# Kernel tuning notes

Measured on AMD Instinct MI355X. Metric: run time of the kernel, lower is better.

The kernel has to match this reference:

```python
import jax, jax.numpy as jnp
import numpy as np

BETA = 0.25  # commitment-loss weight (kwargs['beta'])


def setup_inputs() -> dict:
    key = jax.random.key(0)
    k1, k2 = jax.random.split(key)
    B, C, H, W = 16, 256, 64, 64
    K = 2048
    feats = jax.random.normal(k1, (B, C, H, W), dtype=jnp.float32)
    # nn.Embedding init: uniform(-1/n_codewords, 1/codeword_dim)
    codebook = jax.random.uniform(k2, (K, C), minval=-1.0 / K, maxval=1.0 / C,
                                  dtype=jnp.float32)
    return {"feats": feats, "codebook": codebook}


def reference(feats, codebook):
    B, C, H, W = feats.shape
    K = codebook.shape[0]
    z = jnp.transpose(feats, (0, 2, 3, 1))          # [B,H,W,C]
    zf = z.reshape(-1, C)                            # [N,C], N=B*H*W
    # squared-euclidean distances via ||z||^2 + ||e||^2 - 2 z.e : [N,K]
    d = (jnp.sum(zf * zf, axis=1, keepdims=True)
         + jnp.sum(codebook * codebook, axis=1)
         - 2.0 * (zf @ codebook.T))
    min_encoding_indices = jnp.argmin(d, axis=1)     # [N]
    mat_id_probs = jax.nn.softmax(-jnp.abs(d), axis=1)  # [N,K]
    z_q = codebook[min_encoding_indices].reshape(z.shape)  # [B,H,W,C]
    loss = (BETA * jnp.mean((jax.lax.stop_gradient(z_q) - z) ** 2)
            + jnp.mean((z_q - jax.lax.stop_gradient(z)) ** 2))
    # straight-through estimator
    z_q_st = z + jax.lax.stop_gradient(z_q - z)
    z_q_out = jnp.transpose(z_q_st, (0, 3, 1, 2))    # [B,C,H,W]
    idx_out = min_encoding_indices.reshape(B, H, W)
    probs_out = jnp.transpose(mat_id_probs.reshape(B, H, W, K), (0, 3, 1, 2))
    return z_q_out, idx_out, loss, probs_out
```

## Files before the change

kernel.cpp:

```cpp
#include <hip/hip_runtime.h>

#define HW 4096
#define CC 256
#define KK 2048
#define BB 16
#define NN (BB*HW)

#define ZQ_SZ   (BB*CC*HW)
#define IDX_OFF ZQ_SZ
#define LOSS_OFF (IDX_OFF + NN)
#define PROBS_OFF (LOSS_OFF + 1)

#define EH_OFF 0
#define EE_OFF 262144
#define ZZ_OFF 264192

#define TAU 0.01f
#define CAND_CAP 2048
#define KTC 64
#define KT_N 32

typedef short bf16x8 __attribute__((ext_vector_type(8)));
typedef float f32x16 __attribute__((ext_vector_type(16)));

__device__ __forceinline__ unsigned short bf16rn(float x){
  unsigned u = __float_as_uint(x);
  return (unsigned short)((u + 0x7fffu + ((u >> 16) & 1u)) >> 16);
}

template<int STRIDE>
__device__ __forceinline__ float np_sumsq256(const float* __restrict__ a){
  float res0 = 0.f, res1 = 0.f;
  #pragma unroll
  for (int h = 0; h < 2; h++){
    const float* p = a + (size_t)h * 128 * STRIDE;
    float r[8];
    #pragma unroll
    for (int j = 0; j < 8; j++){ float x = p[(size_t)j * STRIDE]; r[j] = __fmul_rn(x, x); }
    for (int i = 8; i < 128; i += 8){
      #pragma unroll
      for (int j = 0; j < 8; j++){
        float x = p[(size_t)(i + j) * STRIDE];
        r[j] = __fadd_rn(r[j], __fmul_rn(x, x));
      }
    }
    float s = __fadd_rn(__fadd_rn(__fadd_rn(r[0], r[1]), __fadd_rn(r[2], r[3])),
                        __fadd_rn(__fadd_rn(r[4], r[5]), __fadd_rn(r[6], r[7])));
    if (h == 0) res0 = s; else res1 = s;
  }
  return __fadd_rn(res0, res1);
}

__global__ void k_prep2(const float* __restrict__ cb, float* __restrict__ out){
  const int k = blockIdx.x * 256 + threadIdx.x;
  unsigned short* eh = (unsigned short*)(out + EH_OFF);
  const float* row = cb + (size_t)k * CC;
  for (int c = 0; c < CC; c++) eh[k * CC + c] = bf16rn(row[c]);
  out[EE_OFF + k] = np_sumsq256<1>(row);
}

__global__ void k_zz(const float* __restrict__ feats, float* __restrict__ out){
  const int n = blockIdx.x * 256 + threadIdx.x;
  const int b = n >> 12, hw = n & 4095;
  out[ZZ_OFF + n] = np_sumsq256<HW>(feats + (size_t)b * CC * HW + hw);
}

__global__ __launch_bounds__(512, 2)
void k_mfma(const float* __restrict__ feats, const float* __restrict__ cb,
            float* __restrict__ out){
  __shared__ __align__(16) unsigned char lds_e[32768];
  __shared__ float ee_lds[KK];
  __shared__ float pbuf[8448];
  __shared__ unsigned long long rowkey[256];
  __shared__ int cand[CAND_CAP];
  __shared__ int cand_n;
  __shared__ float lsum;

  const int t = threadIdx.x;
  const int w = t >> 6, l = t & 63;
  const int blk = blockIdx.x;
  const int n0 = blk * 256;
  const int bi = n0 >> 12;
  const int hw0 = n0 & 4095;
  const int grp = l >> 5;
  const int code_l = l & 31;
  const int myhw = hw0 + w * 32 + (l & 31);
  const int wb = w * 1056;

  for (int i = t; i < KK; i += 512) ee_lds[i] = out[EE_OFF + i];
  if (t < 256) rowkey[t] = ~0ull;
  if (t == 0){ cand_n = 0; lsum = 0.f; }

  bf16x8 ah[16];
  {
    const float* zb = feats + (size_t)bi * CC * HW + myhw;
    #pragma unroll
    for (int cs = 0; cs < 16; ++cs){
      #pragma unroll
      for (int j = 0; j < 8; ++j){
        int c = cs * 16 + grp * 8 + j;
        ah[cs][j] = (short)bf16rn(zb[(size_t)c * HW]);
      }
    }
  }

  const unsigned short* ehg = (const unsigned short*)(out + EH_OFF);
  float4 stg[4];

#define VLOAD(KT) { \
    _Pragma("unroll") \
    for (int i_ = 0; i_ < 4; ++i_){ \
      int ix_ = i_ * 512 + t; \
      int cd_ = ix_ & 63; \
      int g_  = (ix_ >> 6) & 1; \
      int cs_ = ix_ >> 7; \
      stg[i_] = *(const float4*)(ehg + (size_t)((KT) * KTC + cd_) * CC + cs_ * 16 + g_ * 8); \
    } }

#define DSWRITE() { \
    _Pragma("unroll") \
    for (int i_ = 0; i_ < 4; ++i_) *(float4*)(lds_e + (i_ * 512 + t) * 16) = stg[i_]; }

#define COMPUTE() \
    _Pragma("unroll") \
    for (int ii = 0; ii < 16; ++ii){ accA[ii] = 0.f; accB[ii] = 0.f; accC[ii] = 0.f; accD[ii] = 0.f; } \
    _Pragma("unroll") \
    for (int cs = 0; cs < 16; ++cs){ \
      const unsigned char* bp_ = lds_e + (size_t)(cs * 2 + grp) * 1024 + code_l * 16; \
      bf16x8 b0_ = *(const bf16x8*)(bp_); \
      bf16x8 b1_ = *(const bf16x8*)(bp_ + 512); \
      if (cs & 1){ \
        accB = __builtin_amdgcn_mfma_f32_32x32x16_bf16(ah[cs], b0_, accB, 0, 0, 0); \
        accD = __builtin_amdgcn_mfma_f32_32x32x16_bf16(ah[cs], b1_, accD, 0, 0, 0); \
      } else { \
        accA = __builtin_amdgcn_mfma_f32_32x32x16_bf16(ah[cs], b0_, accA, 0, 0, 0); \
        accC = __builtin_amdgcn_mfma_f32_32x32x16_bf16(ah[cs], b1_, accC, 0, 0, 0); \
      } \
    }

  f32x16 accA, accB, accC, accD;
  float m_[16], sum_[16];
  #pragma unroll
  for (int r = 0; r < 16; ++r){ m_[r] = 3e38f; sum_[r] = 0.f; }

  VLOAD(0);
  for (int kt = 0; kt < KT_N; ++kt){
    __syncthreads();
    DSWRITE();
    __syncthreads();
    if (kt < KT_N - 1) VLOAD(kt + 1);
    COMPUTE();
    float eev0 = ee_lds[kt * KTC + code_l];
    float eev1 = ee_lds[kt * KTC + 32 + code_l];
    #pragma unroll
    for (int r = 0; r < 16; ++r){
      float s0 = eev0 - 2.f * (accA[r] + accB[r]);
      float s1 = eev1 - 2.f * (accC[r] + accD[r]);
      m_[r] = fminf(m_[r], fminf(s0, s1));
      sum_[r] += __expf(-s0) + __expf(-s1);
    }
  }

  #pragma unroll
  for (int r = 0; r < 16; ++r){
    float m = m_[r], ss = sum_[r];
    #pragma unroll
    for (int off = 1; off < 32; off <<= 1){
      m = fminf(m, __shfl_xor(m, off));
      ss += __shfl_xor(ss, off);
    }
    m_[r] = m; sum_[r] = 1.f / ss;
  }

  VLOAD(0);
  for (int kt = 0; kt < KT_N; ++kt){
    __syncthreads();
    DSWRITE();
    __syncthreads();
    if (kt < KT_N - 1) VLOAD(kt + 1);
    COMPUTE();
    float eev0 = ee_lds[kt * KTC + code_l];
    float eev1 = ee_lds[kt * KTC + 32 + code_l];
    const int row = l & 31, hi = l >> 5;
    #pragma unroll
    for (int cf = 0; cf < 2; ++cf){
      #pragma unroll
      for (int r = 0; r < 16; ++r){
        float a = cf ? (accC[r] + accD[r]) : (accA[r] + accB[r]);
        float s = (cf ? eev1 : eev0) - 2.f * a;
        float p = __expf(-s) * sum_[r];
        int rloc = (r & 3) + 8 * (r >> 2) + 4 * grp;
        pbuf[wb + code_l * 33 + rloc] = p;
        if (s <= m_[r] + TAU){
          int slot = atomicAdd(&cand_n, 1);
          if (slot < CAND_CAP) cand[slot] = ((w * 32 + rloc) << 16) | (kt * KTC + cf * 32 + code_l);
        }
      }
      #pragma unroll
      for (int i = 0; i < 16; ++i){
        int codel = 2 * i + hi;
        float pv = pbuf[wb + codel * 33 + row];
        out[(size_t)PROBS_OFF + (size_t)(bi * KK + kt * KTC + cf * 32 + codel) * HW + hw0 + w * 32 + row] = pv;
      }
    }
  }
  __syncthreads();

  int nc = cand_n; if (nc > CAND_CAP) nc = CAND_CAP;
  for (int i = t; i < nc; i += 512){
    int rc = cand[i];
    int rl = rc >> 16, code = rc & 0xffff;
    int n = n0 + rl;
    const float* zp = feats + (size_t)(n >> 12) * CC * HW + (n & 4095);
    const float* ep = cb + (size_t)code * CC;
    float a = 0.f;
    #pragma unroll 8
    for (int c = 0; c < CC; ++c) a = __builtin_fmaf(zp[(size_t)c * HW], ep[c], a);
    float t1 = __fadd_rn(out[ZZ_OFF + n], ee_lds[code]);
    float d = __fadd_rn(t1, -2.f * a);
    unsigned long long key = ((unsigned long long)__float_as_uint(d) << 32) | (unsigned)code;
    atomicMin(&rowkey[rl], key);
  }
  __syncthreads();

  if (t < 256) out[IDX_OFF + n0 + t] = (float)(int)(rowkey[t] & 0xffffffffu);

  {
    int rl = w * 32 + (l & 31);
    int code = (int)(rowkey[rl] & 0xffffffffu);
    const float* ep = cb + (size_t)code * CC;
    int n = n0 + rl;
    const float* zp = feats + (size_t)(n >> 12) * CC * HW + (n & 4095);
    float s = 0.f;
    int c0 = grp * 128;
    for (int c = c0; c < c0 + 128; ++c){
      float dz = ep[c] - zp[(size_t)c * HW];
      s = __builtin_fmaf(dz, dz, s);
    }
    s += __shfl_xor(s, 32);
    if (grp == 0) atomicAdd(&lsum, s);
  }
  __syncthreads();
  if (t == 0) atomicAdd(out + LOSS_OFF, lsum * (1.25f / 16777216.f));
}

__global__ void k_zq(const float* __restrict__ cb, float* __restrict__ out){
  const int f4 = blockIdx.x * 256 + threadIdx.x;
  const int f = f4 * 4;
  const int b = f >> 20;
  const int rem = f & 1048575;
  const int c = rem >> 12;
  const int hw = rem & 4095;
  const int n = b * HW + hw;
  const float* idxf = out + IDX_OFF;
  float4 iv = *(const float4*)(idxf + n);
  float4 o;
  o.x = cb[(size_t)((int)iv.x) * CC + c];
  o.y = cb[(size_t)((int)iv.y) * CC + c];
  o.z = cb[(size_t)((int)iv.z) * CC + c];
  o.w = cb[(size_t)((int)iv.w) * CC + c];
  *(float4*)(out + f) = o;
}

extern "C" void kernel_launch(void* const* d_in, const int* in_sizes, int n_in,
                              void* d_out, int out_size, void* d_ws, size_t ws_size,
                              hipStream_t stream){
  const float* feats = (const float*)d_in[0];
  const float* cb    = (const float*)d_in[1];
  float* out = (float*)d_out;

  (void)hipMemsetAsync(out + LOSS_OFF, 0, sizeof(float), stream);
  hipLaunchKernelGGL(k_prep2, dim3(8),     dim3(256), 0, stream, cb, out);
  hipLaunchKernelGGL(k_zz,    dim3(256),   dim3(256), 0, stream, feats, out);
  hipLaunchKernelGGL(k_mfma,  dim3(256),   dim3(512), 0, stream, feats, cb, out);
  hipLaunchKernelGGL(k_zq,    dim3(16384), dim3(256), 0, stream, cb, out);
}
```

Before: 500.8 us.

## Double-buffer codebook tiles, swap MFMA operands, store probs directly, drop zz kernel

The two passes over codebook tiles are merged into one 64-iteration loop that uses a double-buffered LDS tile, so each iteration needs one barrier instead of two. MFMA operands are swapped so each lane holds a single row's distances, which removes the 32-lane shuffle reductions and the pbuf LDS transpose. Probabilities are written straight to global memory with nontemporal stores. The separate k_zz kernel is removed and ||z||^2 is recomputed per candidate instead. The extra buffer raises LDS use, and the direct stores may coalesce differently than the old transposed writes.

```diff
diff --git a/kernel.cpp b/kernel.cpp
--- a/kernel.cpp
+++ b/kernel.cpp
@@ -13,7 +13,6 @@
 
 #define EH_OFF 0
 #define EE_OFF 262144
-#define ZZ_OFF 264192
 
 #define TAU 0.01f
 #define CAND_CAP 2048
@@ -59,18 +58,11 @@
   out[EE_OFF + k] = np_sumsq256<1>(row);
 }
 
-__global__ void k_zz(const float* __restrict__ feats, float* __restrict__ out){
-  const int n = blockIdx.x * 256 + threadIdx.x;
-  const int b = n >> 12, hw = n & 4095;
-  out[ZZ_OFF + n] = np_sumsq256<HW>(feats + (size_t)b * CC * HW + hw);
-}
-
 __global__ __launch_bounds__(512, 2)
 void k_mfma(const float* __restrict__ feats, const float* __restrict__ cb,
             float* __restrict__ out){
-  __shared__ __align__(16) unsigned char lds_e[32768];
+  __shared__ __align__(16) unsigned char lds_e[2][32768];
   __shared__ float ee_lds[KK];
-  __shared__ float pbuf[8448];
   __shared__ unsigned long long rowkey[256];
   __shared__ int cand[CAND_CAP];
   __shared__ int cand_n;
@@ -78,14 +70,13 @@
 
   const int t = threadIdx.x;
   const int w = t >> 6, l = t & 63;
-  const int blk = blockIdx.x;
-  const int n0 = blk * 256;
+  const int n0 = blockIdx.x * 256;
   const int bi = n0 >> 12;
   const int hw0 = n0 & 4095;
   const int grp = l >> 5;
   const int code_l = l & 31;
-  const int myhw = hw0 + w * 32 + (l & 31);
-  const int wb = w * 1056;
+  const int zrow = l & 31;
+  const int myhw = hw0 + w * 32 + zrow;
 
   for (int i = t; i < KK; i += 512) ee_lds[i] = out[EE_OFF + i];
   if (t < 256) rowkey[t] = ~0ull;
@@ -97,10 +88,8 @@
     #pragma unroll
     for (int cs = 0; cs < 16; ++cs){
       #pragma unroll
-      for (int j = 0; j < 8; ++j){
-        int c = cs * 16 + grp * 8 + j;
-        ah[cs][j] = (short)bf16rn(zb[(size_t)c * HW]);
-      }
+      for (int j = 0; j < 8; ++j)
+        ah[cs][j] = (short)bf16rn(zb[(size_t)(cs * 16 + grp * 8 + j) * HW]);
     }
   }
 
@@ -117,94 +106,71 @@
       stg[i_] = *(const float4*)(ehg + (size_t)((KT) * KTC + cd_) * CC + cs_ * 16 + g_ * 8); \
     } }
 
-#define DSWRITE() { \
-    _Pragma("unroll") \
-    for (int i_ = 0; i_ < 4; ++i_) *(float4*)(lds_e + (i_ * 512 + t) * 16) = stg[i_]; }
-
-#define COMPUTE() \
-    _Pragma("unroll") \
-    for (int ii = 0; ii < 16; ++ii){ accA[ii] = 0.f; accB[ii] = 0.f; accC[ii] = 0.f; accD[ii] = 0.f; } \
+#define DSWRITE(B) { \
+    _Pragma("unroll") \
+    for (int i_ = 0; i_ < 4; ++i_) *(float4*)(&lds_e[B][(i_ * 512 + t) * 16]) = stg[i_]; }
+
+#define COMPUTE(B) { \
+    _Pragma("unroll") \
+    for (int ii = 0; ii < 16; ++ii){ accA[ii] = 0.f; accB[ii] = 0.f; } \
     _Pragma("unroll") \
     for (int cs = 0; cs < 16; ++cs){ \
-      const unsigned char* bp_ = lds_e + (size_t)(cs * 2 + grp) * 1024 + code_l * 16; \
-      bf16x8 b0_ = *(const bf16x8*)(bp_); \
-      bf16x8 b1_ = *(const bf16x8*)(bp_ + 512); \
-      if (cs & 1){ \
-        accB = __builtin_amdgcn_mfma_f32_32x32x16_bf16(ah[cs], b0_, accB, 0, 0, 0); \
-        accD = __builtin_amdgcn_mfma_f32_32x32x16_bf16(ah[cs], b1_, accD, 0, 0, 0); \
-      } else { \
-        accA = __builtin_amdgcn_mfma_f32_32x32x16_bf16(ah[cs], b0_, accA, 0, 0, 0); \
-        accC = __builtin_amdgcn_mfma_f32_32x32x16_bf16(ah[cs], b1_, accC, 0, 0, 0); \
-      } \
-    }
-
-  f32x16 accA, accB, accC, accD;
-  float m_[16], sum_[16];
-  #pragma unroll
-  for (int r = 0; r < 16; ++r){ m_[r] = 3e38f; sum_[r] = 0.f; }
-
-  VLOAD(0);
-  for (int kt = 0; kt < KT_N; ++kt){
+      const unsigned char* bp_ = &lds_e[B][(size_t)(cs * 2 + grp) * 1024 + code_l * 16]; \
+      bf16x8 e0_ = *(const bf16x8*)(bp_); \
+      bf16x8 e1_ = *(const bf16x8*)(bp_ + 512); \
+      accA = __builtin_amdgcn_mfma_f32_32x32x16_bf16(e0_, ah[cs], accA, 0, 0, 0); \
+      accB = __builtin_amdgcn_mfma_f32_32x32x16_bf16(e1_, ah[cs], accB, 0, 0, 0); \
+    } }
+
+  f32x16 accA, accB;
+  float m_ = 3e38f, ss_ = 0.f, inv_ = 0.f;
+
+  VLOAD(0); DSWRITE(0);
+  __syncthreads();
+
+  for (int kt = 0; kt < 2 * KT_N; ++kt){
+    const int tt = kt & 31;
+    const int nb = kt & 1;
+    if (kt < 2 * KT_N - 1) VLOAD((kt + 1) & 31);
+    COMPUTE(nb);
+    const int eebase = tt * 64 + 4 * grp;
+    if (kt < KT_N){
+      #pragma unroll
+      for (int r = 0; r < 16; ++r){
+        int off = (r & 3) + 8 * (r >> 2);
+        float s0 = ee_lds[eebase + off]      - 2.f * accA[r];
+        float s1 = ee_lds[eebase + off + 32] - 2.f * accB[r];
+        m_ = fminf(m_, fminf(s0, s1));
+        ss_ += __expf(-s0) + __expf(-s1);
+      }
+      if (kt == KT_N - 1){
+        m_ = fminf(m_, __shfl_xor(m_, 32));
+        ss_ += __shfl_xor(ss_, 32);
+        inv_ = 1.f / ss_;
+      }
+    } else {
+      #pragma unroll
+      for (int r = 0; r < 16; ++r){
+        int off = (r & 3) + 8 * (r >> 2);
+        int cg = tt * 64 + 4 * grp + off;
+        float s0 = ee_lds[eebase + off]      - 2.f * accA[r];
+        float s1 = ee_lds[eebase + off + 32] - 2.f * accB[r];
+        float* p0 = out + (size_t)PROBS_OFF + (size_t)(bi * KK + cg) * HW + myhw;
+        __builtin_nontemporal_store(__expf(-s0) * inv_, p0);
+        __builtin_nontemporal_store(__expf(-s1) * inv_, p0 + (size_t)32 * HW);
+        if (s0 <= m_ + TAU){
+          int sl = atomicAdd(&cand_n, 1);
+          if (sl < CAND_CAP) cand[sl] = ((w * 32 + zrow) << 16) | cg;
+        }
+        if (s1 <= m_ + TAU){
+          int sl = atomicAdd(&cand_n, 1);
+          if (sl < CAND_CAP) cand[sl] = ((w * 32 + zrow) << 16) | (cg + 32);
+        }
+      }
+    }
+    if (kt < 2 * KT_N - 1) DSWRITE(nb ^ 1);
     __syncthreads();
-    DSWRITE();
-    __syncthreads();
-    if (kt < KT_N - 1) VLOAD(kt + 1);
-    COMPUTE();
-    float eev0 = ee_lds[kt * KTC + code_l];
-    float eev1 = ee_lds[kt * KTC + 32 + code_l];
-    #pragma unroll
-    for (int r = 0; r < 16; ++r){
-      float s0 = eev0 - 2.f * (accA[r] + accB[r]);
-      float s1 = eev1 - 2.f * (accC[r] + accD[r]);
-      m_[r] = fminf(m_[r], fminf(s0, s1));
-      sum_[r] += __expf(-s0) + __expf(-s1);
-    }
-  }
-
-  #pragma unroll
-  for (int r = 0; r < 16; ++r){
-    float m = m_[r], ss = sum_[r];
-    #pragma unroll
-    for (int off = 1; off < 32; off <<= 1){
-      m = fminf(m, __shfl_xor(m, off));
-      ss += __shfl_xor(ss, off);
-    }
-    m_[r] = m; sum_[r] = 1.f / ss;
-  }
-
-  VLOAD(0);
-  for (int kt = 0; kt < KT_N; ++kt){
-    __syncthreads();
-    DSWRITE();
-    __syncthreads();
-    if (kt < KT_N - 1) VLOAD(kt + 1);
-    COMPUTE();
-    float eev0 = ee_lds[kt * KTC + code_l];
-    float eev1 = ee_lds[kt * KTC + 32 + code_l];
-    const int row = l & 31, hi = l >> 5;
-    #pragma unroll
-    for (int cf = 0; cf < 2; ++cf){
-      #pragma unroll
-      for (int r = 0; r < 16; ++r){
-        float a = cf ? (accC[r] + accD[r]) : (accA[r] + accB[r]);
-        float s = (cf ? eev1 : eev0) - 2.f * a;
-        float p = __expf(-s) * sum_[r];
-        int rloc = (r & 3) + 8 * (r >> 2) + 4 * grp;
-        pbuf[wb + code_l * 33 + rloc] = p;
-        if (s <= m_[r] + TAU){
-          int slot = atomicAdd(&cand_n, 1);
-          if (slot < CAND_CAP) cand[slot] = ((w * 32 + rloc) << 16) | (kt * KTC + cf * 32 + code_l);
-        }
-      }
-      #pragma unroll
-      for (int i = 0; i < 16; ++i){
-        int codel = 2 * i + hi;
-        float pv = pbuf[wb + codel * 33 + row];
-        out[(size_t)PROBS_OFF + (size_t)(bi * KK + kt * KTC + cf * 32 + codel) * HW + hw0 + w * 32 + row] = pv;
-      }
-    }
-  }
-  __syncthreads();
+  }
 
   int nc = cand_n; if (nc > CAND_CAP) nc = CAND_CAP;
   for (int i = t; i < nc; i += 512){
@@ -216,7 +182,8 @@
     float a = 0.f;
     #pragma unroll 8
     for (int c = 0; c < CC; ++c) a = __builtin_fmaf(zp[(size_t)c * HW], ep[c], a);
-    float t1 = __fadd_rn(out[ZZ_OFF + n], ee_lds[code]);
+    float zzv = np_sumsq256<HW>(zp);
+    float t1 = __fadd_rn(zzv, ee_lds[code]);
     float d = __fadd_rn(t1, -2.f * a);
     unsigned long long key = ((unsigned long long)__float_as_uint(d) << 32) | (unsigned)code;
     atomicMin(&rowkey[rl], key);
@@ -271,7 +238,6 @@
 
   (void)hipMemsetAsync(out + LOSS_OFF, 0, sizeof(float), stream);
   hipLaunchKernelGGL(k_prep2, dim3(8),     dim3(256), 0, stream, cb, out);
-  hipLaunchKernelGGL(k_zz,    dim3(256),   dim3(256), 0, stream, feats, out);
   hipLaunchKernelGGL(k_mfma,  dim3(256),   dim3(512), 0, stream, feats, cb, out);
   hipLaunchKernelGGL(k_zq,    dim3(16384), dim3(256), 0, stream, cb, out);
 }
```

New measurement: 582.1 us. +16.2%, slower.
